# Optimization experiments

Hardware: AMD Instinct MI355X
Metric: run time of the kernel (lower is better)

Reference implementation:

```python
import jax, jax.numpy as jnp
import numpy as np

EPS = 1.0        # model eps for norm
STEP = 0.05      # step_size

def _norm(x):
    # torch: x / (eps + x.std(-1, keepdims=True)), torch std is unbiased (ddof=1)
    return x / (EPS + jnp.std(x, axis=-1, keepdims=True, ddof=1))

def setup_inputs() -> dict:
    key = jax.random.key(0)
    B, L, LM = 4, 512, 64
    G, E, K, D, KN = 32000, 256, 8, 6, 4
    ks = jax.random.split(key, 16)
    s = lambda k, shape, fan: (jax.random.normal(k, shape, jnp.float32) / np.sqrt(fan)).astype(jnp.float32)
    return dict(
        masked=jax.random.randint(ks[0], (B, L), 0, G),
        unmasked=jax.random.randint(ks[1], (B, L), 0, G),
        mask=jax.random.randint(ks[2], (B, LM), 0, L),
        embed=s(ks[3], (G, E), E),                 # embedding table
        Wt=s(ks[4], (D, E, E), E),                 # transition.weight per layer
        bt=jnp.zeros((D, E), jnp.float32),         # transition.bias per layer
        Wtc=s(ks[5], (D, E, E), E),                # transcore.weight per layer
        Wq=s(ks[6], (D, K * E, E), E),             # attq.weight per layer
        Wd=s(ks[7], (D, K * E, K * E), K * E),     # att_dense.weight per layer
        Wo=s(ks[8], (D, K * E, E), K * E),         # atto.weight per layer
        Wu=s(ks[9], (D, E, E), E),                 # updater.weight per layer
        Wem=s(ks[10], (E, E), E),                  # emittor.weight (head)
        Wkc=s(ks[11], (E * KN, E), E),             # kchoice.weight (head)
        bkc=jnp.zeros((E * KN,), jnp.float32),     # kchoice.bias (head)
    )

def reference(masked, unmasked, mask, embed, Wt, bt, Wtc, Wq, Wd, Wo, Wu, Wem, Wkc, bkc):
    B, L = masked.shape
    G, E = embed.shape
    K = Wq.shape[1] // E
    KN = Wkc.shape[0] // E
    inv_sqrt_e = 1.0 / np.sqrt(E)

    z = _norm(embed[masked])          # [B,L,E] input image
    xsa0 = z

    def step(xsa, p):
        wt, bt_, wtc, wq, wd, wo, wu = p
        # roll-based left/right transitions
        xsad = jax.nn.relu(jnp.roll(xsa, 1, axis=1) @ wt) @ wtc
        xsad = xsad + jax.nn.relu(jnp.roll(xsa, -1, axis=1) @ wtc.T) @ wt.T
        xsad = xsad + z @ wu.T + bt_   # use_input_image
        # QKV_Attention with kernel-expanded head dim: q [B,L,K,E] vs keys/values xsa [B,L,E]
        q = (xsa @ wq.T).reshape(B, L, K, E)
        h = jnp.einsum('blke,bme->blkm', q, xsa) * inv_sqrt_e
        pijk = jax.nn.softmax(h, axis=-1)
        y = jnp.einsum('blkm,bme->blke', pijk, xsa).reshape(B, L, K * E)
        # mode 1: Dense -> Relu -> Dense
        xid = jax.nn.relu(y @ wd.T) @ wo     # [B,L,E]
        xsad = _norm(xsad + xid)             # use_gradnorm
        xsa = _norm(xsa + STEP * xsad)       # use_layernorm
        return xsa, None

    xsa, _ = jax.lax.scan(step, xsa0, (Wt, bt, Wtc, Wq, Wd, Wo, Wu))

    # k-choice loss head (callback_cent)
    LM = mask.shape[1]
    lptok = jnp.take_along_axis(xsa, mask[:, :, None], axis=1)         # [B,LM,E]
    xx = (lptok @ Wkc.T + bkc).reshape(B, LM * KN, E)                  # kchoice
    xx = jnp.einsum('bnl,ble->bne', jnp.einsum('bne,ble->bnl', xx, xsa), xsa)
    logits = (xx @ Wem) @ embed.T                                      # [B,LM*KN,G]
    k_lp = jax.nn.log_softmax(logits, axis=-1).reshape(B, LM, KN, G)
    lptok = jax.scipy.special.logsumexp(k_lp, axis=2) - jnp.log(jnp.float32(KN))
    tgt = jnp.take_along_axis(unmasked, mask, axis=1)                  # [B,LM]
    cent = jnp.take_along_axis(lptok, tgt[:, :, None], axis=-1)[:, :, 0]
    return -cent.mean(-1)                                              # [B]
```

## Files before the change

### kernel.cpp

```cpp
#include <hip/hip_runtime.h>
#include <hip/hip_bf16.h>
#include <math.h>

typedef __bf16 bf16x8 __attribute__((ext_vector_type(8)));
typedef float floatx4 __attribute__((ext_vector_type(4)));

__device__ __forceinline__ short f2b(float f) {
  __hip_bfloat16 h = __float2bfloat16(f);
  return *reinterpret_cast<short*>(&h);
}
__device__ __forceinline__ float b2f(short s) {
  unsigned u = ((unsigned)(unsigned short)s) << 16;
  float f;
  __builtin_memcpy(&f, &u, 4);
  return f;
}

__device__ __forceinline__ void gl2lds16(const void* g, void* l) {
  __builtin_amdgcn_global_load_lds((__attribute__((address_space(1))) const void*)g,
                                   (__attribute__((address_space(3))) void*)l, 16, 0, 0);
}

__device__ __forceinline__ float block_sum(float v, float* sdata) {
#pragma unroll
  for (int o = 32; o > 0; o >>= 1) v += __shfl_down(v, o, 64);
  __syncthreads();
  int lane = threadIdx.x & 63, wid = threadIdx.x >> 6;
  if (lane == 0) sdata[wid] = v;
  __syncthreads();
  float s = 0.f;
  int nw = blockDim.x >> 6;
  for (int i = 0; i < nw; i++) s += sdata[i];
  return s;
}

__global__ void cvt_kernel(const float* __restrict__ src, short* __restrict__ dst, long n4) {
  long i = (long)blockIdx.x * blockDim.x + threadIdx.x;
  if (i < n4) {
    float4 v = ((const float4*)src)[i];
    short4 o;
    o.x = f2b(v.x); o.y = f2b(v.y); o.z = f2b(v.z); o.w = f2b(v.w);
    ((short4*)dst)[i] = o;
  }
}

__global__ void cvt2_kernel(const float* __restrict__ src, short* __restrict__ dst,
                            int ldS, int ldD, long sS, long sD) {
  src += (size_t)blockIdx.z * sS;
  dst += (size_t)blockIdx.z * sD;
  int c = blockIdx.x * 32 + threadIdx.x;
  int r0 = blockIdx.y * 32 + threadIdx.y;
#pragma unroll
  for (int i = 0; i < 32; i += 8)
    dst[(size_t)(r0 + i) * ldD + c] = f2b(src[(size_t)(r0 + i) * ldS + c]);
}

__global__ void cvtT2_kernel(const float* __restrict__ src, short* __restrict__ dst,
                             int ldS, int ldD, long sS, long sD) {
  src += (size_t)blockIdx.z * sS;
  dst += (size_t)blockIdx.z * sD;
  __shared__ float tile[32][33];
  int r0 = blockIdx.y * 32, c0 = blockIdx.x * 32;
  int tx = threadIdx.x, ty = threadIdx.y;
#pragma unroll
  for (int i = 0; i < 32; i += 8)
    tile[ty + i][tx] = src[(size_t)(r0 + ty + i) * ldS + c0 + tx];
  __syncthreads();
#pragma unroll
  for (int i = 0; i < 32; i += 8)
    dst[(size_t)(c0 + ty + i) * ldD + r0 + tx] = f2b(tile[tx][ty + i]);
}

__global__ void embed_norm_kernel(const int* __restrict__ masked,
                                  const float* __restrict__ embed,
                                  float* __restrict__ xsa, short* __restrict__ xsa_bf,
                                  short* __restrict__ xsaT_bf, short* __restrict__ t3,
                                  int E, int L) {
  int row = blockIdx.x;
  int g = masked[row];
  __shared__ float sdata[8];
  float x = embed[(size_t)g * E + threadIdx.x];
  float mean = block_sum(x, sdata) / E;
  float d = x - mean;
  float var = block_sum(d * d, sdata) / (E - 1);
  float val = x / (1.0f + sqrtf(var));
  size_t off = (size_t)row * E + threadIdx.x;
  xsa[off] = val;
  short b = f2b(val);
  xsa_bf[off] = b;
  t3[(size_t)row * 3 * E + 2 * E + threadIdx.x] = b;
  int bb = row / L, l = row - bb * L;
  xsaT_bf[((size_t)bb * E + threadIdx.x) * L + l] = b;
}

template <int BM, int BN, int OUT_BF16>
__global__ __launch_bounds__(256) void bgemm_kernel(
    const short* __restrict__ A, int lda, long sA,
    const short* __restrict__ B, int ldb, long sB,
    void* __restrict__ Cv, int ldc, long sC,
    int Ksz, float alpha, const float* __restrict__ bias,
    int relu, int shiftA, int shiftB, int nsplit, int Lroll) {
  constexpr int WM = BM / 2, WN = BN / 2;
  constexpr int MT = WM / 16, NT = WN / 16;
  constexpr int NCH = (BM + BN) * 8;
  constexpr int LPT = NCH / 256;
  A += (size_t)blockIdx.z * sA;
  B += (size_t)blockIdx.z * sB;
  float* Cf = (float*)Cv + (size_t)blockIdx.z * sC;
  short* Cb = (short*)Cv + (size_t)blockIdx.z * sC;
  int m0 = blockIdx.y * BM, n0 = blockIdx.x * BN;
  int shift = (n0 < nsplit) ? shiftA : shiftB;
  __shared__ short S[2][(BM + BN) * 64];
  int tid = threadIdx.x, lane = tid & 63, w = tid >> 6;
  int wm = (w & 1) * WM, wn = (w >> 1) * WN;
  int ml = lane & 15, q4 = lane >> 4, sw = ml & 7;

  const short* src[LPT];
#pragma unroll
  for (int i = 0; i < LPT; i++) {
    int q = i * 256 + w * 64 + lane;
    if (q < BM * 8) {
      int m = q >> 3, cl = q & 7, cs = cl ^ (m & 7);
      int mg = m0 + m;
      if (shift != 0) {
        int bb = mg / Lroll, l = mg - bb * Lroll;
        l = (l + shift + Lroll) % Lroll;
        mg = bb * Lroll + l;
      }
      src[i] = A + (size_t)mg * lda + cs * 8;
    } else {
      int qb = q - BM * 8;
      int n = qb >> 3, cl = qb & 7, cs = cl ^ (n & 7);
      src[i] = B + (size_t)(n0 + n) * ldb + cs * 8;
    }
  }
#pragma unroll
  for (int i = 0; i < LPT; i++)
    gl2lds16(src[i], &S[0][(i * 256 + w * 64) * 8]);
  floatx4 acc[MT][NT] = {};
  int nT = Ksz >> 6;
  for (int t = 0; t < nT; t++) {
    __syncthreads();
    int cur = t & 1;
    if (t + 1 < nT) {
      int nxt = cur ^ 1, ko = (t + 1) * 64;
#pragma unroll
      for (int i = 0; i < LPT; i++)
        gl2lds16(src[i] + ko, &S[nxt][(i * 256 + w * 64) * 8]);
    }
#pragma unroll
    for (int kk = 0; kk < 2; kk++) {
      int j = kk * 4 + q4;
      bf16x8 af[MT], bg[NT];
#pragma unroll
      for (int mt = 0; mt < MT; mt++) {
        int r = wm + mt * 16 + ml;
        af[mt] = *reinterpret_cast<const bf16x8*>(&S[cur][r * 64 + (j ^ sw) * 8]);
      }
#pragma unroll
      for (int nt = 0; nt < NT; nt++) {
        int r = wn + nt * 16 + ml;
        bg[nt] = *reinterpret_cast<const bf16x8*>(&S[cur][BM * 64 + r * 64 + (j ^ sw) * 8]);
      }
#pragma unroll
      for (int mt = 0; mt < MT; mt++)
#pragma unroll
        for (int nt = 0; nt < NT; nt++)
          acc[mt][nt] = __builtin_amdgcn_mfma_f32_16x16x32_bf16(af[mt], bg[nt], acc[mt][nt], 0, 0, 0);
    }
  }
#pragma unroll
  for (int mt = 0; mt < MT; mt++)
#pragma unroll
    for (int nt = 0; nt < NT; nt++) {
      floatx4 v = acc[mt][nt];
#pragma unroll
      for (int r = 0; r < 4; r++) {
        int grow = m0 + wm + mt * 16 + q4 * 4 + r;
        int gcol = n0 + wn + nt * 16 + ml;
        float x = alpha * v[r];
        if (bias) x += bias[gcol];
        if (relu) x = fmaxf(x, 0.f);
        if (OUT_BF16)
          Cb[(size_t)grow * ldc + gcol] = f2b(x);
        else
          Cf[(size_t)grow * ldc + gcol] = x;
      }
    }
}

__global__ __launch_bounds__(256) void attn_kernel(short* __restrict__ qy,
                                                   const short* __restrict__ kbf,
                                                   const short* __restrict__ vtbf,
                                                   float scale) {
  constexpr int L = 512, E = 256;
  int b = blockIdx.y;
  int m0 = blockIdx.x * 32;
  short* Qg = qy + ((size_t)b * 4096 + m0) * E;
  const short* Kg = kbf + (size_t)b * L * E;
  const short* Vt = vtbf + (size_t)b * E * L;
  __shared__ short LDS[32768];
  int tid = threadIdx.x, lane = tid & 63, w = tid >> 6;
  int ml = lane & 15, q4 = lane >> 4;
  int wm = (w & 1) * 16, wh = w >> 1;
  int wn1 = wh * 256;
  int wn2 = wh * 128;

  bf16x8 af_q[8];
  {
    const short* qsrc = Qg + (size_t)(wm + ml) * E + q4 * 8;
#pragma unroll
    for (int kt = 0; kt < 8; kt++)
      af_q[kt] = *reinterpret_cast<const bf16x8*>(qsrc + kt * 32);
  }

  const short* srcB[8];
#pragma unroll
  for (int i = 0; i < 8; i++) {
    int idx = i * 256 + tid;
    srcB[i] = Kg + (size_t)(idx & 511) * E + (idx >> 9) * 8;
  }
#pragma unroll
  for (int i = 0; i < 8; i++)
    gl2lds16(srcB[i], &LDS[(i * 256 + w * 64) * 8]);

  floatx4 sacc[16] = {};
  for (int kt = 0; kt < 8; kt++) {
    __syncthreads();
    int cur = kt & 1;
    if (kt + 1 < 8) {
      int nxt = cur ^ 1, ko = (kt + 1) * 32;
#pragma unroll
      for (int i = 0; i < 8; i++)
        gl2lds16(srcB[i] + ko, &LDS[nxt * 16384 + (i * 256 + w * 64) * 8]);
    }
    const short* bb = &LDS[cur * 16384];
    bf16x8 a = af_q[kt];
#pragma unroll
    for (int nt = 0; nt < 16; nt++) {
      bf16x8 bg = *reinterpret_cast<const bf16x8*>(bb + (q4 * 512 + wn1 + nt * 16 + ml) * 8);
      sacc[nt] = __builtin_amdgcn_mfma_f32_16x16x32_bf16(a, bg, sacc[nt], 0, 0, 0);
    }
  }
  __syncthreads();

  const short* srcV[4];
#pragma unroll
  for (int i = 0; i < 4; i++) srcV[i] = Vt + (size_t)tid * L + i * 8;
#pragma unroll
  for (int i = 0; i < 4; i++)
    gl2lds16(srcV[i], &LDS[16384 + (i * 256 + w * 64) * 8]);

  float mrow[4] = {-INFINITY, -INFINITY, -INFINITY, -INFINITY};
#pragma unroll
  for (int nt = 0; nt < 16; nt++)
#pragma unroll
    for (int r = 0; r < 4; r++) {
      float v = sacc[nt][r] * scale;
      sacc[nt][r] = v;
      mrow[r] = fmaxf(mrow[r], v);
    }
#pragma unroll
  for (int o = 1; o < 16; o <<= 1)
#pragma unroll
    for (int r = 0; r < 4; r++) mrow[r] = fmaxf(mrow[r], __shfl_xor(mrow[r], o, 64));
  float* stM = (float*)&LDS[24576];
  float* stS = stM + 64;
  if (ml == 0)
#pragma unroll
    for (int r = 0; r < 4; r++) stM[wh * 32 + wm + q4 * 4 + r] = mrow[r];
  __syncthreads();
  float fm[4], ps[4] = {0.f, 0.f, 0.f, 0.f};
#pragma unroll
  for (int r = 0; r < 4; r++)
    fm[r] = fmaxf(stM[wm + q4 * 4 + r], stM[32 + wm + q4 * 4 + r]);
#pragma unroll
  for (int nt = 0; nt < 16; nt++)
#pragma unroll
    for (int r = 0; r < 4; r++) {
      float p = expf(sacc[nt][r] - fm[r]);
      sacc[nt][r] = p;
      ps[r] += p;
    }
#pragma unroll
  for (int o = 1; o < 16; o <<= 1)
#pragma unroll
    for (int r = 0; r < 4; r++) ps[r] += __shfl_xor(ps[r], o, 64);
  if (ml == 0)
#pragma unroll
    for (int r = 0; r < 4; r++) stS[wh * 32 + wm + q4 * 4 + r] = ps[r];
  __syncthreads();
  float inv[4];
#pragma unroll
  for (int r = 0; r < 4; r++)
    inv[r] = 1.f / (stS[wm + q4 * 4 + r] + stS[32 + wm + q4 * 4 + r]);

#pragma unroll
  for (int nt = 0; nt < 16; nt++) {
    int n = wn1 + nt * 16 + ml;
    int base = ((n >> 3) * 32) * 8 + (n & 7);
#pragma unroll
    for (int r = 0; r < 4; r++)
      LDS[base + (wm + q4 * 4 + r) * 8] = f2b(sacc[nt][r] * inv[r]);
  }

  floatx4 oacc[8] = {};
  for (int kc = 0; kc < 16; kc++) {
    __syncthreads();
    int cur = kc & 1;
    if (kc + 1 < 16) {
      int nxt = cur ^ 1, ko = (kc + 1) * 32;
#pragma unroll
      for (int i = 0; i < 4; i++)
        gl2lds16(srcV[i] + ko, &LDS[16384 + nxt * 8192 + (i * 256 + w * 64) * 8]);
    }
    bf16x8 ap = *reinterpret_cast<const bf16x8*>(&LDS[((kc * 4 + q4) * 32 + wm + ml) * 8]);
    const short* vb = &LDS[16384 + cur * 8192];
#pragma unroll
    for (int nt = 0; nt < 8; nt++) {
      bf16x8 bg = *reinterpret_cast<const bf16x8*>(vb + (q4 * 256 + wn2 + nt * 16 + ml) * 8);
      oacc[nt] = __builtin_amdgcn_mfma_f32_16x16x32_bf16(ap, bg, oacc[nt], 0, 0, 0);
    }
  }
#pragma unroll
  for (int nt = 0; nt < 8; nt++)
#pragma unroll
    for (int r = 0; r < 4; r++)
      Qg[(size_t)(wm + q4 * 4 + r) * E + wn2 + nt * 16 + ml] = f2b(oacc[nt][r]);
}

__global__ void addnorm_kernel(const float* __restrict__ xsad,
                               const float* __restrict__ xid,
                               float* __restrict__ xsa, short* __restrict__ xsa_bf,
                               short* __restrict__ xsaT_bf, int E, int L) {
  int row = blockIdx.x, t = threadIdx.x;
  __shared__ float sdata[8];
  size_t off = (size_t)row * E + t;
  float s1 = xsad[off] + xid[off];
  float mean = block_sum(s1, sdata) / E;
  float d = s1 - mean;
  float var = block_sum(d * d, sdata) / (E - 1);
  float n1 = s1 / (1.f + sqrtf(var));
  float t2 = xsa[off] + 0.05f * n1;
  float mean2 = block_sum(t2, sdata) / E;
  float d2 = t2 - mean2;
  float var2 = block_sum(d2 * d2, sdata) / (E - 1);
  float res = t2 / (1.f + sqrtf(var2));
  xsa[off] = res;
  short b = f2b(res);
  xsa_bf[off] = b;
  int bb = row / L, l = row - bb * L;
  xsaT_bf[((size_t)bb * E + t) * L + l] = b;
}

__global__ void gather_kernel(const float* __restrict__ xsa, const int* __restrict__ mask,
                              const int* __restrict__ unmasked,
                              short* __restrict__ lptok_bf, int* __restrict__ tgt,
                              int L, int LM, int E) {
  int bi = blockIdx.x;
  int b = bi / LM;
  int pos = mask[bi];
  float v = xsa[((size_t)b * L + pos) * E + threadIdx.x];
  lptok_bf[(size_t)bi * E + threadIdx.x] = f2b(v);
  if (threadIdx.x == 0) tgt[bi] = unmasked[b * L + pos];
}

__global__ __launch_bounds__(256) void head_stats_kernel(
    const short* __restrict__ V, const short* __restrict__ Eb,
    float* __restrict__ stM, float* __restrict__ stS, int Ksz, int nch) {
  int m0 = blockIdx.y * 128, n0 = blockIdx.x * 128;
  __shared__ short As[2][8192];
  __shared__ short Bs[2][8192];
  int tid = threadIdx.x, lane = tid & 63, w = tid >> 6;
  int wm = (w & 1) * 64, wn = (w >> 1) * 64;
  int ml = lane & 15, q4 = lane >> 4, sw = ml & 7;
  const short* aSrc[4];
  const short* bSrc[4];
#pragma unroll
  for (int i = 0; i < 4; i++) {
    int q = i * 256 + w * 64 + lane;
    int m = q >> 3, cl = q & 7;
    int cs = cl ^ (m & 7);
    aSrc[i] = V + (size_t)(m0 + m) * Ksz + cs * 8;
    bSrc[i] = Eb + (size_t)(n0 + m) * Ksz + cs * 8;
  }
#pragma unroll
  for (int i = 0; i < 4; i++) {
    gl2lds16(aSrc[i], &As[0][(i * 256 + w * 64) * 8]);
    gl2lds16(bSrc[i], &Bs[0][(i * 256 + w * 64) * 8]);
  }
  floatx4 acc[4][4] = {};
  int nT = Ksz >> 6;
  for (int t = 0; t < nT; t++) {
    __syncthreads();
    int cur = t & 1;
    if (t + 1 < nT) {
      int nxt = cur ^ 1, ko = (t + 1) * 64;
#pragma unroll
      for (int i = 0; i < 4; i++) {
        gl2lds16(aSrc[i] + ko, &As[nxt][(i * 256 + w * 64) * 8]);
        gl2lds16(bSrc[i] + ko, &Bs[nxt][(i * 256 + w * 64) * 8]);
      }
    }
#pragma unroll
    for (int kk = 0; kk < 2; kk++) {
      int j = kk * 4 + q4;
      bf16x8 af[4], bg[4];
#pragma unroll
      for (int mt = 0; mt < 4; mt++) {
        int r = wm + mt * 16 + ml;
        af[mt] = *reinterpret_cast<const bf16x8*>(&As[cur][r * 64 + (j ^ sw) * 8]);
      }
#pragma unroll
      for (int nt = 0; nt < 4; nt++) {
        int r = wn + nt * 16 + ml;
        bg[nt] = *reinterpret_cast<const bf16x8*>(&Bs[cur][r * 64 + (j ^ sw) * 8]);
      }
#pragma unroll
      for (int mt = 0; mt < 4; mt++)
#pragma unroll
        for (int nt = 0; nt < 4; nt++)
          acc[mt][nt] = __builtin_amdgcn_mfma_f32_16x16x32_bf16(af[mt], bg[nt], acc[mt][nt], 0, 0, 0);
    }
  }
  __syncthreads();
  float (*sred)[2] = (float (*)[2]) & As[0][0];
  float (*sred2)[2] = (float (*)[2]) & Bs[0][0];
  float mx[4][4];
#pragma unroll
  for (int mt = 0; mt < 4; mt++)
#pragma unroll
    for (int r = 0; r < 4; r++)
      mx[mt][r] = fmaxf(fmaxf(acc[mt][0][r], acc[mt][1][r]), fmaxf(acc[mt][2][r], acc[mt][3][r]));
#pragma unroll
  for (int off = 1; off < 16; off <<= 1)
#pragma unroll
    for (int mt = 0; mt < 4; mt++)
#pragma unroll
      for (int r = 0; r < 4; r++) mx[mt][r] = fmaxf(mx[mt][r], __shfl_xor(mx[mt][r], off, 64));
  if (ml == 0)
#pragma unroll
    for (int mt = 0; mt < 4; mt++)
#pragma unroll
      for (int r = 0; r < 4; r++) sred[wm + mt * 16 + q4 * 4 + r][w >> 1] = mx[mt][r];
  __syncthreads();
  float sm[4][4];
#pragma unroll
  for (int mt = 0; mt < 4; mt++)
#pragma unroll
    for (int r = 0; r < 4; r++) {
      int row = wm + mt * 16 + q4 * 4 + r;
      float fm = fmaxf(sred[row][0], sred[row][1]);
      float s = 0.f;
#pragma unroll
      for (int nt = 0; nt < 4; nt++) s += expf(acc[mt][nt][r] - fm);
      sm[mt][r] = s;
    }
#pragma unroll
  for (int off = 1; off < 16; off <<= 1)
#pragma unroll
    for (int mt = 0; mt < 4; mt++)
#pragma unroll
      for (int r = 0; r < 4; r++) sm[mt][r] += __shfl_xor(sm[mt][r], off, 64);
  if (ml == 0)
#pragma unroll
    for (int mt = 0; mt < 4; mt++)
#pragma unroll
      for (int r = 0; r < 4; r++) sred2[wm + mt * 16 + q4 * 4 + r][w >> 1] = sm[mt][r];
  __syncthreads();
  if (tid < 128) {
    float fm = fmaxf(sred[tid][0], sred[tid][1]);
    stM[(size_t)(m0 + tid) * nch + blockIdx.x] = fm;
    stS[(size_t)(m0 + tid) * nch + blockIdx.x] = sred2[tid][0] + sred2[tid][1];
  }
}

__global__ void lse_reduce_kernel(const float* __restrict__ statsM,
                                  const float* __restrict__ statsS,
                                  float* __restrict__ lse, int nch) {
  int row = blockIdx.x, t = threadIdx.x;
  float m = -INFINITY, s = 0.f;
  for (int c = t; c < nch; c += blockDim.x) {
    float cm = statsM[(size_t)row * nch + c];
    float cs = statsS[(size_t)row * nch + c];
    float M = fmaxf(m, cm);
    s = s * expf(m - M) + cs * expf(cm - M);
    m = M;
  }
  __shared__ float sm[256], ss[256];
  sm[t] = m;
  ss[t] = s;
  __syncthreads();
  for (int o = 128; o > 0; o >>= 1) {
    if (t < o) {
      float m2 = sm[t + o], s2 = ss[t + o];
      float M = fmaxf(sm[t], m2);
      float sc = ss[t] * expf(sm[t] - M) + s2 * expf(m2 - M);
      sm[t] = M;
      ss[t] = sc;
    }
    __syncthreads();
  }
  if (t == 0) lse[row] = sm[0] + logf(ss[0]);
}

__global__ void logit_tgt_kernel(const short* __restrict__ V, const short* __restrict__ Eb,
                                 const int* __restrict__ tgt, float* __restrict__ lt,
                                 int E, int Nn, int KN, int LM) {
  int row = blockIdx.x;
  int b = row / Nn;
  int i = (row - b * Nn) / KN;
  int g = tgt[b * LM + i];
  __shared__ float sdata[8];
  float v = b2f(V[(size_t)row * E + threadIdx.x]) * b2f(Eb[(size_t)g * E + threadIdx.x]);
  float s = block_sum(v, sdata);
  if (threadIdx.x == 0) lt[row] = s;
}

__global__ void final_kernel(const float* __restrict__ lt, const float* __restrict__ lse,
                             float* __restrict__ out, int LM, int KN) {
  int b = blockIdx.x, i = threadIdx.x;
  int base = (b * LM + i) * KN;
  float m = -INFINITY;
  for (int k = 0; k < KN; k++) m = fmaxf(m, lt[base + k] - lse[base + k]);
  float s = 0.f;
  for (int k = 0; k < KN; k++) s += expf(lt[base + k] - lse[base + k] - m);
  float cent = m + logf(s) - logf((float)KN);
#pragma unroll
  for (int o = 32; o > 0; o >>= 1) cent += __shfl_down(cent, o, 64);
  if (i == 0) out[b] = -cent / LM;
}

static inline void bgemm(hipStream_t st, int cfg, const short* A, int lda, long sA,
                         const short* B, int ldb, long sB,
                         void* C, int ldc, long sC, int M, int N, int Ksz, int nb,
                         float alpha, const float* bias, int relu, int out_bf16,
                         int shiftA, int shiftB, int nsplit, int Lroll) {
  dim3 block(256);
  if (cfg == 0) {
    dim3 grid(N / 128, M / 128, nb);
    if (out_bf16)
      bgemm_kernel<128, 128, 1><<<grid, block, 0, st>>>(A, lda, sA, B, ldb, sB, C, ldc, sC, Ksz, alpha, bias, relu, shiftA, shiftB, nsplit, Lroll);
    else
      bgemm_kernel<128, 128, 0><<<grid, block, 0, st>>>(A, lda, sA, B, ldb, sB, C, ldc, sC, Ksz, alpha, bias, relu, shiftA, shiftB, nsplit, Lroll);
  } else if (cfg == 1) {
    dim3 grid(N / 64, M / 128, nb);
    if (out_bf16)
      bgemm_kernel<128, 64, 1><<<grid, block, 0, st>>>(A, lda, sA, B, ldb, sB, C, ldc, sC, Ksz, alpha, bias, relu, shiftA, shiftB, nsplit, Lroll);
    else
      bgemm_kernel<128, 64, 0><<<grid, block, 0, st>>>(A, lda, sA, B, ldb, sB, C, ldc, sC, Ksz, alpha, bias, relu, shiftA, shiftB, nsplit, Lroll);
  } else {
    dim3 grid(N / 64, M / 64, nb);
    if (out_bf16)
      bgemm_kernel<64, 64, 1><<<grid, block, 0, st>>>(A, lda, sA, B, ldb, sB, C, ldc, sC, Ksz, alpha, bias, relu, shiftA, shiftB, nsplit, Lroll);
    else
      bgemm_kernel<64, 64, 0><<<grid, block, 0, st>>>(A, lda, sA, B, ldb, sB, C, ldc, sC, Ksz, alpha, bias, relu, shiftA, shiftB, nsplit, Lroll);
  }
}

static inline void cvt(hipStream_t st, const float* src, short* dst, long n) {
  long n4 = n / 4;
  cvt_kernel<<<(int)((n4 + 255) / 256), 256, 0, st>>>(src, dst, n4);
}

static inline void cvt2(hipStream_t st, const float* src, short* dst, int R, int C,
                        int ldS, int ldD, long sS, long sD, int nb) {
  dim3 grid(C / 32, R / 32, nb), block(32, 8);
  cvt2_kernel<<<grid, block, 0, st>>>(src, dst, ldS, ldD, sS, sD);
}

static inline void cvtT2(hipStream_t st, const float* src, short* dst, int R, int C,
                         int ldS, int ldD, long sS, long sD, int nb) {
  dim3 grid(C / 32, R / 32, nb), block(32, 8);
  cvtT2_kernel<<<grid, block, 0, st>>>(src, dst, ldS, ldD, sS, sD);
}

extern "C" void kernel_launch(void* const* d_in, const int* in_sizes, int n_in,
                              void* d_out, int out_size, void* d_ws, size_t ws_size,
                              hipStream_t stream) {
  const int* masked = (const int*)d_in[0];
  const int* unmasked = (const int*)d_in[1];
  const int* mask = (const int*)d_in[2];
  const float* embed = (const float*)d_in[3];
  const float* Wt = (const float*)d_in[4];
  const float* bt = (const float*)d_in[5];
  const float* Wtc = (const float*)d_in[6];
  const float* Wq = (const float*)d_in[7];
  const float* Wd = (const float*)d_in[8];
  const float* Wo = (const float*)d_in[9];
  const float* Wu = (const float*)d_in[10];
  const float* Wem = (const float*)d_in[11];
  const float* Wkc = (const float*)d_in[12];
  const float* bkc = (const float*)d_in[13];

  const int B = out_size;
  const int BL = in_sizes[0];
  const int L = BL / B;
  const int BLM = in_sizes[2];
  const int LM = BLM / B;
  const int E = in_sizes[4] / in_sizes[5];
  const int D = in_sizes[5] / E;
  const int G = in_sizes[3] / E;
  const int K = in_sizes[7] / (D * E * E);
  const int KN = in_sizes[12] / (E * E);
  const int KE = K * E;
  const int N = LM * KN;
  const float inv_sqrt_e = 1.0f / sqrtf((float)E);
  const int nch = G / 128;
  const int E3 = 3 * E;

  char* base = (char*)d_ws;
  size_t off = 0;
  auto carve = [&](size_t bytes) {
    char* p = base + off;
    off += (bytes + 255) & ~(size_t)255;
    return p;
  };
  float* xsa = (float*)carve((size_t)BL * E * 4);
  float* xsad = (float*)carve((size_t)BL * E * 4);
  float* xid = (float*)carve((size_t)BL * E * 4);
  float* stM = (float*)carve((size_t)B * N * nch * 4);
  float* stS = (float*)carve((size_t)B * N * nch * 4);
  float* lse = (float*)carve((size_t)B * N * 4);
  float* lt = (float*)carve((size_t)B * N * 4);
  int* tgt = (int*)carve((size_t)B * LM * 4);
  short* xsa_bf = (short*)carve((size_t)BL * E * 2);
  short* xsaT_bf = (short*)carve((size_t)B * E * L * 2);
  short* t3 = (short*)carve((size_t)BL * E3 * 2);
  short* qy_bf = (short*)carve((size_t)BL * KE * 2);
  short* r_bf = (short*)carve((size_t)B * L * K * L * 2);
  short* wd_all = (short*)carve((size_t)D * KE * KE * 2);
  short* wq_all = (short*)carve((size_t)D * KE * E * 2);
  short* woT_all = (short*)carve((size_t)D * E * KE * 2);
  short* Bcat1 = (short*)carve((size_t)D * 2 * E * E * 2);
  short* Bcat2 = (short*)carve((size_t)D * E * E3 * 2);
  short* embed_bf = (short*)carve((size_t)G * E * 2);
  short* WemT_bf = (short*)carve((size_t)E * E * 2);
  short* Wkc_bf = (short*)carve((size_t)KN * E * E * 2);
  short* gram_bf = (short*)carve((size_t)B * E * E * 2);
  short* xx_bf = (short*)carve((size_t)B * N * E * 2);
  short* xx2_bf = (short*)carve((size_t)B * N * E * 2);
  short* vv_bf = (short*)carve((size_t)B * N * E * 2);
  short* lptok_bf = (short*)carve((size_t)BLM * E * 2);

  cvt(stream, embed, embed_bf, (long)G * E);
  cvt(stream, Wd, wd_all, (long)D * KE * KE);
  cvt(stream, Wq, wq_all, (long)D * KE * E);
  cvt(stream, Wkc, Wkc_bf, (long)KN * E * E);
  cvtT2(stream, Wem, WemT_bf, E, E, E, E, 0, 0, 1);
  cvtT2(stream, Wo, woT_all, KE, E, E, KE, (long)KE * E, (long)E * KE, D);
  cvtT2(stream, Wt, Bcat1, E, E, E, E, (long)E * E, (long)2 * E * E, D);
  cvt2(stream, Wtc, Bcat1 + (size_t)E * E, E, E, E, E, (long)E * E, (long)2 * E * E, D);
  cvtT2(stream, Wtc, Bcat2, E, E, E, E3, (long)E * E, (long)E * E3, D);
  cvt2(stream, Wt, Bcat2 + E, E, E, E, E3, (long)E * E, (long)E * E3, D);
  cvt2(stream, Wu, Bcat2 + 2 * E, E, E, E, E3, (long)E * E, (long)E * E3, D);

  embed_norm_kernel<<<BL, E, 0, stream>>>(masked, embed, xsa, xsa_bf, xsaT_bf, t3, E, L);

  for (int d = 0; d < D; d++) {
    const float* btl = bt + (size_t)d * E;
    bgemm(stream, 2, xsa_bf, E, 0, Bcat1 + (size_t)d * 2 * E * E, E, 0,
          t3, E3, 0, BL, 2 * E, E, 1, 1.f, nullptr, 1, 1, -1, +1, E, L);
    bgemm(stream, 2, t3, E3, 0, Bcat2 + (size_t)d * E * E3, E3, 0,
          xsad, E, 0, BL, E, E3, 1, 1.f, btl, 0, 0, 0, 0, 0, L);
    bgemm(stream, 1, xsa_bf, E, 0, wq_all + (size_t)d * KE * E, E, 0,
          qy_bf, KE, 0, BL, KE, E, 1, 1.f, nullptr, 0, 1, 0, 0, 0, L);
    attn_kernel<<<dim3(L * K / 32, B), 256, 0, stream>>>(qy_bf, xsa_bf, xsaT_bf, inv_sqrt_e);
    bgemm(stream, 1, qy_bf, KE, 0, wd_all + (size_t)d * KE * KE, KE, 0,
          r_bf, KE, 0, BL, KE, KE, 1, 1.f, nullptr, 1, 1, 0, 0, 0, L);
    bgemm(stream, 2, r_bf, KE, 0, woT_all + (size_t)d * E * KE, KE, 0,
          xid, E, 0, BL, E, KE, 1, 1.f, nullptr, 0, 0, 0, 0, 0, L);
    addnorm_kernel<<<BL, E, 0, stream>>>(xsad, xid, xsa, xsa_bf, xsaT_bf, E, L);
  }

  gather_kernel<<<BLM, E, 0, stream>>>(xsa, mask, unmasked, lptok_bf, tgt, L, LM, E);
  bgemm(stream, 2, xsaT_bf, L, (long)E * L, xsaT_bf, L, (long)E * L,
        gram_bf, E, (long)E * E, E, E, L, B, 1.f, nullptr, 0, 1, 0, 0, 0, L);
  bgemm(stream, 2, lptok_bf, E, 0, Wkc_bf, E, 0, xx_bf, KN * E, 0, BLM, KN * E, E, 1,
        1.f, bkc, 0, 1, 0, 0, 0, L);
  bgemm(stream, 2, xx_bf, E, (long)N * E, gram_bf, E, (long)E * E,
        xx2_bf, E, (long)N * E, N, E, E, B, 1.f, nullptr, 0, 1, 0, 0, 0, L);
  bgemm(stream, 2, xx2_bf, E, 0, WemT_bf, E, 0, vv_bf, E, 0, B * N, E, E, 1,
        1.f, nullptr, 0, 1, 0, 0, 0, L);
  head_stats_kernel<<<dim3(nch, (B * N) / 128), 256, 0, stream>>>(vv_bf, embed_bf, stM, stS, E, nch);
  lse_reduce_kernel<<<B * N, 256, 0, stream>>>(stM, stS, lse, nch);
  logit_tgt_kernel<<<B * N, E, 0, stream>>>(vv_bf, embed_bf, tgt, lt, E, N, KN, LM);
  final_kernel<<<B, LM, 0, stream>>>(lt, lse, (float*)d_out, LM, KN);
}
```

Baseline: 1.073 ms.

## Load attention K and V operands directly from global memory instead of LDS staging

The attention kernel no longer stages K and V tiles into double-buffered LDS through global_load_lds with per-iteration barriers. Each wave now reads its MFMA B operands straight from global memory (expected to hit in L2, since each batch's K and V are shared by many blocks), and LDS is cut to the P tile plus small softmax-statistic arrays. This removes the barriers and copy overhead in both matmul loops and reduces LDS use, which may allow higher occupancy. The cost is strided, less coalesced global reads, and the two waves that share a column half now fetch the same K/V data separately.

```diff
diff --git a/kernel.cpp b/kernel.cpp
--- a/kernel.cpp
+++ b/kernel.cpp
@@ -199,7 +199,9 @@
   short* Qg = qy + ((size_t)b * 4096 + m0) * E;
   const short* Kg = kbf + (size_t)b * L * E;
   const short* Vt = vtbf + (size_t)b * E * L;
-  __shared__ short LDS[32768];
+  __shared__ short Pl[16384];
+  __shared__ float stM[2][32];
+  __shared__ float stS[2][32];
   int tid = threadIdx.x, lane = tid & 63, w = tid >> 6;
   int ml = lane & 15, q4 = lane >> 4;
   int wm = (w & 1) * 16, wh = w >> 1;
@@ -214,42 +216,18 @@
       af_q[kt] = *reinterpret_cast<const bf16x8*>(qsrc + kt * 32);
   }
 
-  const short* srcB[8];
-#pragma unroll
-  for (int i = 0; i < 8; i++) {
-    int idx = i * 256 + tid;
-    srcB[i] = Kg + (size_t)(idx & 511) * E + (idx >> 9) * 8;
-  }
-#pragma unroll
-  for (int i = 0; i < 8; i++)
-    gl2lds16(srcB[i], &LDS[(i * 256 + w * 64) * 8]);
-
   floatx4 sacc[16] = {};
+  const short* kbase = Kg + (size_t)(wn1 + ml) * E + q4 * 8;
+#pragma unroll 2
   for (int kt = 0; kt < 8; kt++) {
-    __syncthreads();
-    int cur = kt & 1;
-    if (kt + 1 < 8) {
-      int nxt = cur ^ 1, ko = (kt + 1) * 32;
-#pragma unroll
-      for (int i = 0; i < 8; i++)
-        gl2lds16(srcB[i] + ko, &LDS[nxt * 16384 + (i * 256 + w * 64) * 8]);
-    }
-    const short* bb = &LDS[cur * 16384];
+    const short* kb = kbase + kt * 32;
     bf16x8 a = af_q[kt];
 #pragma unroll
     for (int nt = 0; nt < 16; nt++) {
-      bf16x8 bg = *reinterpret_cast<const bf16x8*>(bb + (q4 * 512 + wn1 + nt * 16 + ml) * 8);
+      bf16x8 bg = *reinterpret_cast<const bf16x8*>(kb + (size_t)nt * 16 * E);
       sacc[nt] = __builtin_amdgcn_mfma_f32_16x16x32_bf16(a, bg, sacc[nt], 0, 0, 0);
     }
   }
-  __syncthreads();
-
-  const short* srcV[4];
-#pragma unroll
-  for (int i = 0; i < 4; i++) srcV[i] = Vt + (size_t)tid * L + i * 8;
-#pragma unroll
-  for (int i = 0; i < 4; i++)
-    gl2lds16(srcV[i], &LDS[16384 + (i * 256 + w * 64) * 8]);
 
   float mrow[4] = {-INFINITY, -INFINITY, -INFINITY, -INFINITY};
 #pragma unroll
@@ -264,16 +242,14 @@
   for (int o = 1; o < 16; o <<= 1)
 #pragma unroll
     for (int r = 0; r < 4; r++) mrow[r] = fmaxf(mrow[r], __shfl_xor(mrow[r], o, 64));
-  float* stM = (float*)&LDS[24576];
-  float* stS = stM + 64;
   if (ml == 0)
 #pragma unroll
-    for (int r = 0; r < 4; r++) stM[wh * 32 + wm + q4 * 4 + r] = mrow[r];
+    for (int r = 0; r < 4; r++) stM[wh][wm + q4 * 4 + r] = mrow[r];
   __syncthreads();
   float fm[4], ps[4] = {0.f, 0.f, 0.f, 0.f};
 #pragma unroll
   for (int r = 0; r < 4; r++)
-    fm[r] = fmaxf(stM[wm + q4 * 4 + r], stM[32 + wm + q4 * 4 + r]);
+    fm[r] = fmaxf(stM[0][wm + q4 * 4 + r], stM[1][wm + q4 * 4 + r]);
 #pragma unroll
   for (int nt = 0; nt < 16; nt++)
 #pragma unroll
@@ -288,37 +264,32 @@
     for (int r = 0; r < 4; r++) ps[r] += __shfl_xor(ps[r], o, 64);
   if (ml == 0)
 #pragma unroll
-    for (int r = 0; r < 4; r++) stS[wh * 32 + wm + q4 * 4 + r] = ps[r];
+    for (int r = 0; r < 4; r++) stS[wh][wm + q4 * 4 + r] = ps[r];
   __syncthreads();
   float inv[4];
 #pragma unroll
   for (int r = 0; r < 4; r++)
-    inv[r] = 1.f / (stS[wm + q4 * 4 + r] + stS[32 + wm + q4 * 4 + r]);
+    inv[r] = 1.f / (stS[0][wm + q4 * 4 + r] + stS[1][wm + q4 * 4 + r]);
 
 #pragma unroll
   for (int nt = 0; nt < 16; nt++) {
     int n = wn1 + nt * 16 + ml;
-    int base = ((n >> 3) * 32) * 8 + (n & 7);
+    int base = (n >> 3) * 256 + (n & 7);
 #pragma unroll
     for (int r = 0; r < 4; r++)
-      LDS[base + (wm + q4 * 4 + r) * 8] = f2b(sacc[nt][r] * inv[r]);
-  }
+      Pl[base + (wm + q4 * 4 + r) * 8] = f2b(sacc[nt][r] * inv[r]);
+  }
+  __syncthreads();
 
   floatx4 oacc[8] = {};
+  const short* vbase = Vt + (size_t)(wn2 + ml) * L + q4 * 8;
+#pragma unroll 2
   for (int kc = 0; kc < 16; kc++) {
-    __syncthreads();
-    int cur = kc & 1;
-    if (kc + 1 < 16) {
-      int nxt = cur ^ 1, ko = (kc + 1) * 32;
-#pragma unroll
-      for (int i = 0; i < 4; i++)
-        gl2lds16(srcV[i] + ko, &LDS[16384 + nxt * 8192 + (i * 256 + w * 64) * 8]);
-    }
-    bf16x8 ap = *reinterpret_cast<const bf16x8*>(&LDS[((kc * 4 + q4) * 32 + wm + ml) * 8]);
-    const short* vb = &LDS[16384 + cur * 8192];
+    bf16x8 ap = *reinterpret_cast<const bf16x8*>(&Pl[((kc * 4 + q4) * 32 + wm + ml) * 8]);
+    const short* vb = vbase + kc * 32;
 #pragma unroll
     for (int nt = 0; nt < 8; nt++) {
-      bf16x8 bg = *reinterpret_cast<const bf16x8*>(vb + (q4 * 256 + wn2 + nt * 16 + ml) * 8);
+      bf16x8 bg = *reinterpret_cast<const bf16x8*>(vb + (size_t)nt * 16 * L);
       oacc[nt] = __builtin_amdgcn_mfma_f32_16x16x32_bf16(ap, bg, oacc[nt], 0, 0, 0);
     }
   }
```

New measurement: 1.311 ms. +22.2%, slower.
